# Performance work log

Hardware: AMD Instinct MI355X
Metric: run time of the kernel (lower is better)

The kernel has to match this reference:

```python
import jax, jax.numpy as jnp
import numpy as np

N_HEADS = 16
WINDOW = 4
THETA = 10000.0


def _freqs_1d(dim, L, theta=THETA):
    f = 1.0 / theta ** (np.arange(0, dim, 2, dtype=np.float32) / dim)  # [dim/2]
    ang = np.arange(L, dtype=np.float32)[:, None] * f[None, :]         # [L, dim/2]
    return jnp.asarray(np.cos(ang)), jnp.asarray(np.sin(ang))


def _freqs_2d(dim, H, W, theta=THETA):
    f = 1.0 / theta ** (np.arange(0, dim, 2, dtype=np.float32) / dim)  # [dim/2]
    fh = np.arange(H, dtype=np.float32)[:, None] * f[0::2][None, :]    # [H, dim/4]
    fw = np.arange(W, dtype=np.float32)[:, None] * f[1::2][None, :]    # [W, dim/4]
    ang = np.concatenate([
        np.broadcast_to(fh[:, None, :], (H, W, fh.shape[1])),
        np.broadcast_to(fw[None, :, :], (H, W, fw.shape[1])),
    ], axis=-1)                                                        # [H, W, dim/2]
    return jnp.asarray(np.cos(ang)), jnp.asarray(np.sin(ang))


def _rope(x, cos, sin):
    # x: [..., N, D]; cos/sin broadcastable to x's leading dims with trailing D/2
    sh = x.shape
    xr = x.reshape(sh[:-1] + (sh[-1] // 2, 2))
    re, im = xr[..., 0], xr[..., 1]
    o_re = re * cos - im * sin
    o_im = re * sin + im * cos
    return jnp.stack([o_re, o_im], axis=-1).reshape(sh)


def setup_inputs() -> dict:
    key = jax.random.key(0)
    ks = jax.random.split(key, 5)
    B, T, H, W, E = 2, 8, 16, 16, 512
    S = 2 * T * H * W
    std = 0.02
    return {
        "hidden_states": jax.random.normal(ks[0], (B, S, E), jnp.float32),
        "in_proj_weight": jax.random.normal(ks[1], (3 * E, E), jnp.float32) * std,
        "in_proj_bias": jnp.zeros((3 * E,), jnp.float32),
        "out_proj_weight": jax.random.normal(ks[2], (E, E), jnp.float32) * std,
        "out_proj_bias": jnp.zeros((E,), jnp.float32),
        "temporal_embed": jax.random.normal(ks[3], (WINDOW, E), jnp.float32) * std,
        "T": T, "H": H, "W": W,
    }


def reference(hidden_states, in_proj_weight, in_proj_bias, out_proj_weight,
              out_proj_bias, temporal_embed, T, H, W):
    B, S, E = hidden_states.shape
    n, d = N_HEADS, E // N_HEADS
    HW = H * W
    THW = T * HW
    L2 = 2 * HW  # tokens per frame fed to attention

    # first (outer) in-projection
    qkv = hidden_states @ in_proj_weight.T + in_proj_bias  # [B,S,3E]
    q, k, v = jnp.split(qkv, 3, axis=-1)
    q = q.reshape(B, S, n, d)
    k = k.reshape(B, S, n, d)

    # 1D RoPE on first T*H*W tokens (per-frame length H*W)
    cos1, sin1 = _freqs_1d(d, HW)
    c1, s1 = cos1[:, None, :], sin1[:, None, :]  # [HW,1,d/2]
    q1 = _rope(q[:, :THW].reshape(B * T, HW, n, d), c1, s1)
    k1 = _rope(k[:, :THW].reshape(B * T, HW, n, d), c1, s1)

    # 2D RoPE on last T*H*W tokens
    cos2, sin2 = _freqs_2d(d, H, W)
    c2, s2 = cos2[:, :, None, :], sin2[:, :, None, :]  # [H,W,1,d/2]
    q2 = _rope(q[:, THW:].reshape(B * T, H, W, n, d), c2, s2).reshape(B * T, HW, n, d)
    k2 = _rope(k[:, THW:].reshape(B * T, H, W, n, d), c2, s2).reshape(B * T, HW, n, d)

    q_mha = jnp.concatenate([q1, q2], axis=1).reshape(B * T, L2, E)
    k_comb = jnp.concatenate([k1, k2], axis=1).reshape(B, T, L2, E)
    v_comb = v.reshape(B, T, L2, E)

    # sliding window over frames (left-pad with zeros)
    k_pad = jnp.pad(k_comb, ((0, 0), (WINDOW - 1, 0), (0, 0), (0, 0)))
    v_pad = jnp.pad(v_comb, ((0, 0), (WINDOW - 1, 0), (0, 0), (0, 0)))
    k_win = jnp.stack([k_pad[:, i:i + T] for i in range(WINDOW)], axis=2)
    v_win = jnp.stack([v_pad[:, i:i + T] for i in range(WINDOW)], axis=2)
    k_win = k_win + temporal_embed[None, None, :, None, :]
    k_mha = k_win.reshape(B * T, WINDOW * L2, E)
    v_mha = v_win.reshape(B * T, WINDOW * L2, E)

    # inner nn.MultiheadAttention: projects q/k/v AGAIN with in_proj chunks
    Wq, Wk, Wv = jnp.split(in_proj_weight, 3, axis=0)
    bq, bk, bv = jnp.split(in_proj_bias, 3, axis=0)
    qh = (q_mha @ Wq.T + bq).reshape(B * T, L2, n, d)
    kh = (k_mha @ Wk.T + bk).reshape(B * T, WINDOW * L2, n, d)
    vh = (v_mha @ Wv.T + bv).reshape(B * T, WINDOW * L2, n, d)

    scale = 1.0 / jnp.sqrt(jnp.asarray(d, jnp.float32))
    scores = jnp.einsum('bqnd,bknd->bnqk', qh, kh) * scale
    attn = jax.nn.softmax(scores, axis=-1)
    o = jnp.einsum('bnqk,bknd->bqnd', attn, vh).reshape(B * T, L2, E)
    out = o @ out_proj_weight.T + out_proj_bias
    return out.reshape(B, S, E)
```

## Files before the change

kernel.cpp:

```cpp
#include <hip/hip_runtime.h>


#define LOG2T_OVER_16 0.83048202372184059f
#define SCL 0.25505837391169026f

typedef unsigned short u16;
typedef unsigned int u32;
typedef __attribute__((ext_vector_type(2))) unsigned int u32x2;
typedef __attribute__((ext_vector_type(4))) float f32x4;
typedef __attribute__((ext_vector_type(8))) short s16x8;

__device__ __forceinline__ u16 bf16b(float x) {
  u32 u = __float_as_uint(x);
  u32 r = u + 0x7FFFu + ((u >> 16) & 1u);
  return (u16)(r >> 16);
}
__device__ __forceinline__ float bf2f(u16 s) {
  return __uint_as_float(((u32)s) << 16);
}
__device__ __forceinline__ u32 cvtpk(float lo, float hi) {
  u32 r;
  asm("v_cvt_pk_bf16_f32 %0, %1, %2" : "=v"(r) : "v"(lo), "v"(hi));
  return r;
}

__device__ __forceinline__ void gld_lds16(const u16* g, u16* l) {
  __builtin_amdgcn_global_load_lds(
      (const __attribute__((address_space(1))) unsigned int*)g,
      (__attribute__((address_space(3))) unsigned int*)l, 16, 0, 0);
}

__global__ __launch_bounds__(256) void cast3_bf16(
    const float* __restrict__ a, const float* __restrict__ b,
    const float* __restrict__ c, u16* __restrict__ dst) {
  const int i = blockIdx.x * 256 + threadIdx.x;
  const float* s;
  int so;
  if (i < 524288) { s = a; so = i; }
  else if (i < 622592) { s = b; so = i - 524288; }
  else { s = c; so = i - 622592; }
  float4 x = ((const float4*)s)[so * 2], y = ((const float4*)s)[so * 2 + 1];
  union { u32 u[4]; s16x8 v; } w;
  w.u[0] = cvtpk(x.x, x.y); w.u[1] = cvtpk(x.z, x.w);
  w.u[2] = cvtpk(y.x, y.y); w.u[3] = cvtpk(y.z, y.w);
  ((s16x8*)dst)[i] = w.v;
}

template<int OUTF32>
__device__ __forceinline__ void gemm_core(
    const u16* __restrict__ A, const u16* __restrict__ Bw,
    const float* __restrict__ bias, void* __restrict__ Cp,
    int N, int K, float scale, u16* As, u16* Bs) {
  const int tid = threadIdx.x;
  const int row0 = blockIdx.y * 128;
  const int col0 = blockIdx.x * 128;
  const int lane = tid & 63, wid = tid >> 6;
  const int col = lane & 15, g = lane >> 4;
  const int wm = wid >> 1, wn = wid & 1;

  const int s0 = tid, s1 = 256 + tid;
  const int r0 = s0 >> 2, kp0 = (s0 & 3) * 8;
  const int r1 = s1 >> 2, kp1 = (s1 & 3) * 8;

  f32x4 acc[4][4] = {};

  auto stage = [&](int buf, int k0) {
    u16* ab = As + buf * 4096;
    u16* bb = Bs + buf * 4096;
    gld_lds16(A + (size_t)(row0 + r0) * K + k0 + kp0, ab + s0 * 8);
    gld_lds16(A + (size_t)(row0 + r1) * K + k0 + kp1, ab + s1 * 8);
    gld_lds16(Bw + (size_t)(col0 + r0) * K + k0 + kp0, bb + s0 * 8);
    gld_lds16(Bw + (size_t)(col0 + r1) * K + k0 + kp1, bb + s1 * 8);
  };

  stage(0, 0);
  asm volatile("s_waitcnt vmcnt(0)" ::: "memory");
  __syncthreads();

  const int NT = K / 32;
  int cur = 0;
  for (int t = 0; t < NT; ++t) {
    if (t + 1 < NT) stage(cur ^ 1, (t + 1) * 32);
    const u16* ab = As + cur * 4096;
    const u16* bb = Bs + cur * 4096;
    s16x8 a[4], b[4];
    #pragma unroll
    for (int i = 0; i < 4; ++i)
      a[i] = *(const s16x8*)(ab + (wm * 64 + i * 16 + col) * 32 + g * 8);
    #pragma unroll
    for (int i = 0; i < 4; ++i)
      b[i] = *(const s16x8*)(bb + (wn * 64 + i * 16 + col) * 32 + g * 8);
    #pragma unroll
    for (int mi = 0; mi < 4; ++mi)
      #pragma unroll
      for (int ni = 0; ni < 4; ++ni)
        acc[mi][ni] = __builtin_amdgcn_mfma_f32_16x16x32_bf16(a[mi], b[ni], acc[mi][ni], 0, 0, 0);
    asm volatile("s_waitcnt vmcnt(0)" ::: "memory");
    __syncthreads();
    cur ^= 1;
  }

  const int crow = row0 + wm * 64, ccol = col0 + wn * 64;
  #pragma unroll
  for (int mi = 0; mi < 4; ++mi) {
    #pragma unroll
    for (int ni = 0; ni < 4; ++ni) {
      const int cc = ccol + ni * 16 + col;
      const float bb_ = bias ? bias[cc] : 0.0f;
      #pragma unroll
      for (int r = 0; r < 4; ++r) {
        const int rr = crow + mi * 16 + g * 4 + r;
        float v = (acc[mi][ni][r] + bb_) * scale;
        if (OUTF32) ((float*)Cp)[(size_t)rr * N + cc] = v;
        else        ((u16*)Cp)[(size_t)rr * N + cc] = bf16b(v);
      }
    }
  }
}

__global__ __launch_bounds__(256) void gemm_bf16(
    const u16* __restrict__ A, const u16* __restrict__ Bw,
    const float* __restrict__ bias, u16* __restrict__ C, int N, int K, float scale) {
  __shared__ u16 As[2 * 4096];
  __shared__ u16 Bs[2 * 4096];
  gemm_core<0>(A, Bw, bias, C, N, K, scale, As, Bs);
}

__global__ __launch_bounds__(256) void gemm_f32out(
    const u16* __restrict__ A, const u16* __restrict__ Bw,
    const float* __restrict__ bias, float* __restrict__ C, int N, int K, float scale) {
  __shared__ u16 As[2 * 4096];
  __shared__ u16 Bs[2 * 4096];
  gemm_core<1>(A, Bw, bias, C, N, K, scale, As, Bs);
}

__global__ __launch_bounds__(256) void gemm2_batched(
    const u16* __restrict__ Ab, const u16* __restrict__ Wb,
    const float* __restrict__ b_in, u16* __restrict__ Cb) {
  __shared__ u16 As[2 * 4096];
  __shared__ u16 Bs[2 * 4096];
  const int z = blockIdx.z;
  const u16* A  = Ab + (size_t)z * 4194304;
  const u16* Bw = Wb + (size_t)z * 262144;
  u16* C = Cb + (size_t)z * 4194304;
  const float* bias = (z == 0) ? b_in : (z == 2 ? b_in + 1024 : nullptr);
  const float scale = (z == 0) ? SCL : 1.0f;
  gemm_core<0>(A, Bw, bias, C, 512, 512, scale, As, Bs);
}

__global__ __launch_bounds__(256) void ang_table_kernel(float2* __restrict__ tab) {
  const int idx = blockIdx.x * 256 + threadIdx.x;
  const int j = idx >> 4, u = idx & 15;
  float ang;
  if (j < 256) {
    ang = (float)j * exp2f(-(float)u * LOG2T_OVER_16);
  } else {
    const int jj = j - 256, hh = jj >> 4, ww = jj & 15;
    ang = (u < 8) ? (float)hh * exp2f(-(float)(2 * u) * LOG2T_OVER_16)
                  : (float)ww * exp2f(-(float)(2 * (u - 8) + 1) * LOG2T_OVER_16);
  }
  float s, c;
  sincosf(ang, &s, &c);
  tab[idx] = make_float2(c, s);
}

__global__ __launch_bounds__(256) void rope_relayout_bf(
    const u16* __restrict__ qkv, const float2* __restrict__ tab,
    u16* __restrict__ qm, u16* __restrict__ kc, u16* __restrict__ vc) {
  const int R = blockIdx.x * 2 + (threadIdx.x >> 7);
  const int t2 = threadIdx.x & 127;
  const int j = R & 511, bt = R >> 9;
  const int b = bt >> 3, tt = bt & 7;
  const int head = t2 >> 3, u0 = (t2 & 7) * 2;
  const int e0 = head * 32 + u0 * 2;

  const int tok = (j < 256) ? (b * 4096 + tt * 256 + j)
                            : (b * 4096 + 2048 + tt * 256 + (j - 256));
  float4 cs = *(const float4*)&tab[j * 16 + u0];
  const float c0 = cs.x, s0 = cs.y, c1 = cs.z, s1 = cs.w;

  const size_t base = (size_t)tok * 1536 + e0;
  const size_t orow = (size_t)R * 512 + e0;

  auto rot = [&](u32x2 in) -> u32x2 {
    float r0 = bf2f((u16)(in[0] & 0xffff)), i0 = bf2f((u16)(in[0] >> 16));
    float r1 = bf2f((u16)(in[1] & 0xffff)), i1 = bf2f((u16)(in[1] >> 16));
    u32x2 o;
    o[0] = cvtpk(r0 * c0 - i0 * s0, r0 * s0 + i0 * c0);
    o[1] = cvtpk(r1 * c1 - i1 * s1, r1 * s1 + i1 * c1);
    return o;
  };
  *(u32x2*)(qm + orow) = rot(*(const u32x2*)(qkv + base));
  *(u32x2*)(kc + orow) = rot(*(const u32x2*)(qkv + base + 512));
  const int vtok = b * 4096 + tt * 512 + j;
  *(u32x2*)(vc + orow) = *(const u32x2*)(qkv + (size_t)vtok * 1536 + 1024 + e0);
}

__global__ __launch_bounds__(256) void tep_kernel(
    const float* __restrict__ te, const float* __restrict__ Wk,
    const float* __restrict__ bk, float* __restrict__ tep) {
  const int idx = blockIdx.x * 256 + threadIdx.x;
  const int i = idx >> 9, c = idx & 511;
  float s = bk[c];
  const float* terow = te + i * 512;
  const float* wrow = Wk + (size_t)c * 512;
  #pragma unroll 8
  for (int e = 0; e < 512; ++e) s = fmaf(terow[e], wrow[e], s);
  tep[idx] = s;
}

__global__ __launch_bounds__(256) void transpose_v_bf16(
    const u16* __restrict__ vc2, u16* __restrict__ vt) {
  const int f = blockIdx.x, h = blockIdx.y;
  __shared__ float tile[64][35];
  const int tid = threadIdx.x;
  for (int k0 = 0; k0 < 512; k0 += 64) {
    __syncthreads();
    {
      const int key = tid >> 2, d0 = (tid & 3) * 8;
      s16x8 v = *(const s16x8*)(vc2 + (size_t)(f * 512 + k0 + key) * 512 + h * 32 + d0);
      #pragma unroll
      for (int q = 0; q < 8; ++q) tile[key][d0 + q] = bf2f((u16)v[q]);
    }
    __syncthreads();
    {
      const int d = tid >> 3, j0 = (tid & 7) * 8;
      union { u32 u[4]; s16x8 v; } w;
      #pragma unroll
      for (int q = 0; q < 4; ++q)
        w.u[q] = cvtpk(tile[j0 + 2 * q][d], tile[j0 + 2 * q + 1][d]);
      *(s16x8*)(vt + (size_t)((f * 16 + h) * 32 + d) * 512 + k0 + j0) = w.v;
    }
  }
}

__global__ __launch_bounds__(256) void attn_mfma(
    const u16* __restrict__ qh, const u16* __restrict__ kbf,
    const float* __restrict__ tep, const u16* __restrict__ vt,
    const float* __restrict__ bv, u16* __restrict__ obf) {
  const u32 orig = blockIdx.x;
  const u32 sw = (orig & 7) * 256 + (orig >> 3);
  const int h = sw >> 7, bt = (sw >> 3) & 15, zc = sw & 7;
  const int b = bt >> 3, t = bt & 7;
  const int tid = threadIdx.x;
  const int lane = tid & 63, w = tid >> 6;
  const int col = lane & 15, g = lane >> 4;

  __shared__ __align__(128) u16 plds[4][4096];
  u16* pl = plds[w];
  const u32 pl_base = (u32)(uintptr_t)pl + (u32)lane * 8u;
  float* cf = (float*)&plds[0][0];

  const int phys_e = (col & 4) ? 4 + (col >> 3) : (col >> 3);
  const int wbase = phys_e * 64 + (col & 3) * 16 + g * 4;

  const int qrow0 = bt * 512 + zc * 64;
  s16x8 qa[4];
  #pragma unroll
  for (int m = 0; m < 4; ++m)
    qa[m] = *(const s16x8*)(qh + (size_t)(qrow0 + m * 16 + col) * 512 + h * 32 + g * 8);

  f32x4 acc[4][2] = {};
  f32x4 lsum[4] = {};
  const f32x4 zero4 = {0.f, 0.f, 0.f, 0.f};

  const int fs = t + w - 3;
  const float* tprow = tep + w * 512 + h * 32;
  float t8[8];
  #pragma unroll
  for (int j = 0; j < 8; ++j) t8[j] = tprow[g * 8 + j];

  if (fs < 0) {
    float* pf = (float*)pl;
    #pragma unroll
    for (int m = 0; m < 4; ++m) {
      float part = 0.f;
      #pragma unroll
      for (int j = 0; j < 8; ++j) part = fmaf(bf2f((u16)qa[m][j]), t8[j], part);
      part += __shfl_xor(part, 16);
      part += __shfl_xor(part, 32);
      float e = __builtin_amdgcn_exp2f(part) * 512.0f;
      if (lane < 16) pf[m * 16 + col] = e;
    }
    asm volatile("s_waitcnt lgkmcnt(0)" ::: "memory");
    const float bv0 = bv[h * 32 + col], bv1 = bv[h * 32 + 16 + col];
    #pragma unroll
    for (int m = 0; m < 4; ++m)
      #pragma unroll
      for (int r = 0; r < 4; ++r) {
        float e = pf[m * 16 + g * 4 + r];
        lsum[m][r] += (col == 0) ? e : 0.f;
        acc[m][0][r] += e * bv0;
        acc[m][1][r] += e * bv1;
      }
  } else {
    const size_t krow0 = (size_t)((b * 8 + fs) * 512);
    const size_t vrow0 = (size_t)(((b * 8 + fs) * 16 + h) * 32);
    for (int it = 0; it < 8; ++it) {
      const int kk0 = it * 64;
      f32x4 S[4][4];
      #pragma unroll
      for (int n = 0; n < 4; ++n) {
        s16x8 kv = *(const s16x8*)(kbf + (krow0 + kk0 + n * 16 + col) * 512 + h * 32 + g * 8);
        union { u32 u[4]; s16x8 v; } kb;
        #pragma unroll
        for (int p = 0; p < 4; ++p)
          kb.u[p] = cvtpk(bf2f((u16)kv[2 * p]) + t8[2 * p],
                          bf2f((u16)kv[2 * p + 1]) + t8[2 * p + 1]);
        #pragma unroll
        for (int m = 0; m < 4; ++m)
          S[m][n] = __builtin_amdgcn_mfma_f32_16x16x32_bf16(qa[m], kb.v, zero4, 0, 0, 0);
      }
      #pragma unroll
      for (int m = 0; m < 4; ++m) {
        #pragma unroll
        for (int n = 0; n < 4; ++n) {
          f32x4 p;
          #pragma unroll
          for (int r = 0; r < 4; ++r) p[r] = __builtin_amdgcn_exp2f(S[m][n][r]);
          lsum[m] += p;
          const int E = m * 1024 + (n >> 1) * 512 + (n & 1) * 128 + wbase;
          *(uint2*)&pl[E] = make_uint2(cvtpk(p[0], p[1]), cvtpk(p[2], p[3]));
        }
      }
      s16x8 vfr[2][2];
      #pragma unroll
      for (int ks = 0; ks < 2; ++ks)
        #pragma unroll
        for (int n = 0; n < 2; ++n)
          vfr[ks][n] = *(const s16x8*)(vt + (vrow0 + n * 16 + col) * 512 + kk0 + ks * 32 + g * 8);
      asm volatile("s_waitcnt lgkmcnt(0)" ::: "memory");
      union AF { u32x2 h2[2]; s16x8 v; };
      AF pa[4][2];
      #pragma unroll
      for (int m = 0; m < 4; ++m)
        #pragma unroll
        for (int ks = 0; ks < 2; ++ks) {
          u32 a0 = pl_base + (u32)((m * 1024 + ks * 512) * 2);
          asm volatile("ds_read_b64_tr_b16 %0, %1" : "=v"(pa[m][ks].h2[0]) : "v"(a0));
          asm volatile("ds_read_b64_tr_b16 %0, %1 offset:512" : "=v"(pa[m][ks].h2[1]) : "v"(a0));
        }
      asm volatile("s_waitcnt lgkmcnt(0)" ::: "memory");
      __builtin_amdgcn_sched_barrier(0);
      #pragma unroll
      for (int m = 0; m < 4; ++m)
        #pragma unroll
        for (int ks = 0; ks < 2; ++ks)
          #pragma unroll
          for (int n = 0; n < 2; ++n)
            acc[m][n] = __builtin_amdgcn_mfma_f32_16x16x32_bf16(pa[m][ks].v, vfr[ks][n], acc[m][n], 0, 0, 0);
    }
  }

  #pragma unroll
  for (int m = 0; m < 4; ++m)
    #pragma unroll
    for (int r = 0; r < 4; ++r) {
      float s = lsum[m][r];
      s += __shfl_xor(s, 1);
      s += __shfl_xor(s, 2);
      s += __shfl_xor(s, 4);
      s += __shfl_xor(s, 8);
      lsum[m][r] = s;
    }

  __syncthreads();
  if (w > 0) {
    float* dst = cf + (size_t)(w - 1) * 2048 + lane * 32;
    #pragma unroll
    for (int m = 0; m < 4; ++m) {
      *(f32x4*)(dst + m * 8) = acc[m][0];
      *(f32x4*)(dst + m * 8 + 4) = acc[m][1];
    }
    if (col == 0) {
      float* d2 = cf + 6144 + (w - 1) * 64 + g * 16;
      #pragma unroll
      for (int m = 0; m < 4; ++m) *(f32x4*)(d2 + m * 4) = lsum[m];
    }
  }
  __syncthreads();
  if (w == 0) {
    #pragma unroll
    for (int w2 = 0; w2 < 3; ++w2) {
      const float* src = cf + (size_t)w2 * 2048 + lane * 32;
      const float* s2 = cf + 6144 + w2 * 64 + g * 16;
      #pragma unroll
      for (int m = 0; m < 4; ++m) {
        acc[m][0] += *(const f32x4*)(src + m * 8);
        acc[m][1] += *(const f32x4*)(src + m * 8 + 4);
        lsum[m] += *(const f32x4*)(s2 + m * 4);
      }
    }
    #pragma unroll
    for (int m = 0; m < 4; ++m) {
      f32x4 inv;
      #pragma unroll
      for (int r = 0; r < 4; ++r) inv[r] = 1.0f / lsum[m][r];
      #pragma unroll
      for (int n = 0; n < 2; ++n)
        #pragma unroll
        for (int r = 0; r < 4; ++r)
          pl[(m * 16 + g * 4 + r) * 32 + n * 16 + col] = bf16b(acc[m][n][r] * inv[r]);
    }
    asm volatile("s_waitcnt lgkmcnt(0)" ::: "memory");
    #pragma unroll
    for (int i = 0; i < 8; ++i) {
      const int row = i * 8 + (lane >> 3);
      u32x2 wv = *(u32x2*)&pl[row * 32 + (lane & 7) * 4];
      *(u32x2*)(obf + (size_t)(qrow0 + row) * 512 + h * 32 + (lane & 7) * 4) = wv;
    }
  }
}

extern "C" void kernel_launch(void* const* d_in, const int* in_sizes, int n_in,
                              void* d_out, int out_size, void* d_ws, size_t ws_size,
                              hipStream_t stream) {
  (void)in_sizes; (void)n_in; (void)out_size; (void)ws_size;
  const float* hs    = (const float*)d_in[0];
  const float* w_in  = (const float*)d_in[1];
  const float* b_in  = (const float*)d_in[2];
  const float* w_out = (const float*)d_in[3];
  const float* b_out = (const float*)d_in[4];
  const float* te    = (const float*)d_in[5];

  u16* w16 = (u16*)d_ws;
  u16* hs_bf   = w16;
  u16* win_bf  = w16 + 4194304;
  u16* wout_bf = w16 + 4980736;
  u16* qkv_bf  = w16 + 5242880;
  u16* qm_bf   = w16 + 17825792;
  u16* kc_bf   = w16 + 22020096;
  u16* vc_bf   = w16 + 26214400;
  float* tep   = (float*)(w16 + 30408704);
  float2* tab  = (float2*)(w16 + 30412800);
  u16* qh_bf   = w16 + 5242880;
  u16* kbf     = w16 + 9437184;
  u16* vc2_bf  = w16 + 13631488;
  u16* vt      = w16 + 17825792;
  u16* o_bf    = w16 + 22020096;

  cast3_bf16<<<2560, 256, 0, stream>>>(hs, w_in, w_out, w16);
  ang_table_kernel<<<32, 256, 0, stream>>>(tab);

  gemm_bf16<<<dim3(12, 64), 256, 0, stream>>>(hs_bf, win_bf, b_in, qkv_bf, 1536, 512, 1.0f);

  rope_relayout_bf<<<4096, 256, 0, stream>>>(qkv_bf, tab, qm_bf, kc_bf, vc_bf);

  tep_kernel<<<8, 256, 0, stream>>>(te, w_in + 512 * 512, b_in + 512, tep);

  gemm2_batched<<<dim3(4, 64, 3), 256, 0, stream>>>(qm_bf, win_bf, b_in, qh_bf);

  transpose_v_bf16<<<dim3(16, 16), 256, 0, stream>>>(vc2_bf, vt);

  attn_mfma<<<2048, 256, 0, stream>>>(qh_bf, kbf, tep, vt, b_in + 1024, o_bf);

  gemm_f32out<<<dim3(4, 64), 256, 0, stream>>>(o_bf, wout_bf, b_out, (float*)d_out, 512, 512, 1.0f);
}
```

Before: 274.5 us.

## Fuse V transpose into gemm epilogue and restructure attention to 512-thread blocks

```diff
diff --git a/kernel.cpp b/kernel.cpp
--- a/kernel.cpp
+++ b/kernel.cpp
@@ -46,11 +46,11 @@
   ((s16x8*)dst)[i] = w.v;
 }
 
-template<int OUTF32>
+template<int MODE>
 __device__ __forceinline__ void gemm_core(
     const u16* __restrict__ A, const u16* __restrict__ Bw,
     const float* __restrict__ bias, void* __restrict__ Cp,
-    int N, int K, float scale, u16* As, u16* Bs) {
+    int N, int K, int lda, float scale, u16* As, u16* Bs) {
   const int tid = threadIdx.x;
   const int row0 = blockIdx.y * 128;
   const int col0 = blockIdx.x * 128;
@@ -67,8 +67,8 @@
   auto stage = [&](int buf, int k0) {
     u16* ab = As + buf * 4096;
     u16* bb = Bs + buf * 4096;
-    gld_lds16(A + (size_t)(row0 + r0) * K + k0 + kp0, ab + s0 * 8);
-    gld_lds16(A + (size_t)(row0 + r1) * K + k0 + kp1, ab + s1 * 8);
+    gld_lds16(A + (size_t)(row0 + r0) * lda + k0 + kp0, ab + s0 * 8);
+    gld_lds16(A + (size_t)(row0 + r1) * lda + k0 + kp1, ab + s1 * 8);
     gld_lds16(Bw + (size_t)(col0 + r0) * K + k0 + kp0, bb + s0 * 8);
     gld_lds16(Bw + (size_t)(col0 + r1) * K + k0 + kp1, bb + s1 * 8);
   };
@@ -107,12 +107,22 @@
     for (int ni = 0; ni < 4; ++ni) {
       const int cc = ccol + ni * 16 + col;
       const float bb_ = bias ? bias[cc] : 0.0f;
-      #pragma unroll
-      for (int r = 0; r < 4; ++r) {
-        const int rr = crow + mi * 16 + g * 4 + r;
-        float v = (acc[mi][ni][r] + bb_) * scale;
-        if (OUTF32) ((float*)Cp)[(size_t)rr * N + cc] = v;
-        else        ((u16*)Cp)[(size_t)rr * N + cc] = bf16b(v);
+      if (MODE == 2) {
+        const int key0 = crow + mi * 16 + g * 4;
+        u16* dst = (u16*)Cp +
+            ((size_t)((key0 >> 9) * 16 + (cc >> 5)) * 32 + (cc & 31)) * 512 + (key0 & 511);
+        union { u16 s[4]; u32x2 v; } pk;
+        #pragma unroll
+        for (int r = 0; r < 4; ++r) pk.s[r] = bf16b(acc[mi][ni][r] + bb_);
+        *(u32x2*)dst = pk.v;
+      } else {
+        #pragma unroll
+        for (int r = 0; r < 4; ++r) {
+          const int rr = crow + mi * 16 + g * 4 + r;
+          float v = (acc[mi][ni][r] + bb_) * scale;
+          if (MODE == 1) ((float*)Cp)[(size_t)rr * N + cc] = v;
+          else           ((u16*)Cp)[(size_t)rr * N + cc] = bf16b(v);
+        }
       }
     }
   }
@@ -123,7 +133,7 @@
     const float* __restrict__ bias, u16* __restrict__ C, int N, int K, float scale) {
   __shared__ u16 As[2 * 4096];
   __shared__ u16 Bs[2 * 4096];
-  gemm_core<0>(A, Bw, bias, C, N, K, scale, As, Bs);
+  gemm_core<0>(A, Bw, bias, C, N, K, K, scale, As, Bs);
 }
 
 __global__ __launch_bounds__(256) void gemm_f32out(
@@ -131,21 +141,25 @@
     const float* __restrict__ bias, float* __restrict__ C, int N, int K, float scale) {
   __shared__ u16 As[2 * 4096];
   __shared__ u16 Bs[2 * 4096];
-  gemm_core<1>(A, Bw, bias, C, N, K, scale, As, Bs);
+  gemm_core<1>(A, Bw, bias, C, N, K, K, scale, As, Bs);
 }
 
 __global__ __launch_bounds__(256) void gemm2_batched(
-    const u16* __restrict__ Ab, const u16* __restrict__ Wb,
-    const float* __restrict__ b_in, u16* __restrict__ Cb) {
+    const u16* __restrict__ Ab, const u16* __restrict__ qkv,
+    const u16* __restrict__ Wb, const float* __restrict__ b_in,
+    u16* __restrict__ Cb) {
   __shared__ u16 As[2 * 4096];
   __shared__ u16 Bs[2 * 4096];
   const int z = blockIdx.z;
-  const u16* A  = Ab + (size_t)z * 4194304;
   const u16* Bw = Wb + (size_t)z * 262144;
   u16* C = Cb + (size_t)z * 4194304;
-  const float* bias = (z == 0) ? b_in : (z == 2 ? b_in + 1024 : nullptr);
-  const float scale = (z == 0) ? SCL : 1.0f;
-  gemm_core<0>(A, Bw, bias, C, 512, 512, scale, As, Bs);
+  if (z == 2) {
+    gemm_core<2>(qkv + 1024, Bw, b_in + 1024, C, 512, 512, 1536, 1.0f, As, Bs);
+  } else {
+    const float* bias = (z == 0) ? b_in : nullptr;
+    const float scale = (z == 0) ? SCL : 1.0f;
+    gemm_core<0>(Ab + (size_t)z * 4194304, Bw, bias, C, 512, 512, 512, scale, As, Bs);
+  }
 }
 
 __global__ __launch_bounds__(256) void ang_table_kernel(float2* __restrict__ tab) {
@@ -166,7 +180,7 @@
 
 __global__ __launch_bounds__(256) void rope_relayout_bf(
     const u16* __restrict__ qkv, const float2* __restrict__ tab,
-    u16* __restrict__ qm, u16* __restrict__ kc, u16* __restrict__ vc) {
+    u16* __restrict__ qm, u16* __restrict__ kc) {
   const int R = blockIdx.x * 2 + (threadIdx.x >> 7);
   const int t2 = threadIdx.x & 127;
   const int j = R & 511, bt = R >> 9;
@@ -192,8 +206,6 @@
   };
   *(u32x2*)(qm + orow) = rot(*(const u32x2*)(qkv + base));
   *(u32x2*)(kc + orow) = rot(*(const u32x2*)(qkv + base + 512));
-  const int vtok = b * 4096 + tt * 512 + j;
-  *(u32x2*)(vc + orow) = *(const u32x2*)(qkv + (size_t)vtok * 1536 + 1024 + e0);
 }
 
 __global__ __launch_bounds__(256) void tep_kernel(
@@ -209,32 +221,7 @@
   tep[idx] = s;
 }
 
-__global__ __launch_bounds__(256) void transpose_v_bf16(
-    const u16* __restrict__ vc2, u16* __restrict__ vt) {
-  const int f = blockIdx.x, h = blockIdx.y;
-  __shared__ float tile[64][35];
-  const int tid = threadIdx.x;
-  for (int k0 = 0; k0 < 512; k0 += 64) {
-    __syncthreads();
-    {
-      const int key = tid >> 2, d0 = (tid & 3) * 8;
-      s16x8 v = *(const s16x8*)(vc2 + (size_t)(f * 512 + k0 + key) * 512 + h * 32 + d0);
-      #pragma unroll
-      for (int q = 0; q < 8; ++q) tile[key][d0 + q] = bf2f((u16)v[q]);
-    }
-    __syncthreads();
-    {
-      const int d = tid >> 3, j0 = (tid & 7) * 8;
-      union { u32 u[4]; s16x8 v; } w;
-      #pragma unroll
-      for (int q = 0; q < 4; ++q)
-        w.u[q] = cvtpk(tile[j0 + 2 * q][d], tile[j0 + 2 * q + 1][d]);
-      *(s16x8*)(vt + (size_t)((f * 16 + h) * 32 + d) * 512 + k0 + j0) = w.v;
-    }
-  }
-}
-
-__global__ __launch_bounds__(256) void attn_mfma(
+__global__ __launch_bounds__(512) void attn_mfma(
     const u16* __restrict__ qh, const u16* __restrict__ kbf,
     const float* __restrict__ tep, const u16* __restrict__ vt,
     const float* __restrict__ bv, u16* __restrict__ obf) {
@@ -243,171 +230,155 @@
   const int h = sw >> 7, bt = (sw >> 3) & 15, zc = sw & 7;
   const int b = bt >> 3, t = bt & 7;
   const int tid = threadIdx.x;
-  const int lane = tid & 63, w = tid >> 6;
+  const int lane = tid & 63, wv = tid >> 6;
+  const int slot = wv & 3, half = wv >> 2;
   const int col = lane & 15, g = lane >> 4;
 
-  __shared__ __align__(128) u16 plds[4][4096];
-  u16* pl = plds[w];
-  const u32 pl_base = (u32)(uintptr_t)pl + (u32)lane * 8u;
-  float* cf = (float*)&plds[0][0];
-
-  const int phys_e = (col & 4) ? 4 + (col >> 3) : (col >> 3);
-  const int wbase = phys_e * 64 + (col & 3) * 16 + g * 4;
-
-  const int qrow0 = bt * 512 + zc * 64;
-  s16x8 qa[4];
+  __shared__ float cf[6400];
+
+  const int qrow0 = bt * 512 + zc * 64 + half * 32;
+  s16x8 qa[2];
   #pragma unroll
-  for (int m = 0; m < 4; ++m)
+  for (int m = 0; m < 2; ++m)
     qa[m] = *(const s16x8*)(qh + (size_t)(qrow0 + m * 16 + col) * 512 + h * 32 + g * 8);
 
-  f32x4 acc[4][2] = {};
-  f32x4 lsum[4] = {};
-  const f32x4 zero4 = {0.f, 0.f, 0.f, 0.f};
-
-  const int fs = t + w - 3;
-  const float* tprow = tep + w * 512 + h * 32;
+  const float* tprow = tep + slot * 512 + h * 32;
   float t8[8];
   #pragma unroll
   for (int j = 0; j < 8; ++j) t8[j] = tprow[g * 8 + j];
-
+  float dtc[2];
+  #pragma unroll
+  for (int m = 0; m < 2; ++m) {
+    float p = 0.f;
+    #pragma unroll
+    for (int j = 0; j < 8; ++j) p = fmaf(bf2f((u16)qa[m][j]), t8[j], p);
+    p += __shfl_xor(p, 16);
+    p += __shfl_xor(p, 32);
+    dtc[m] = p;
+  }
+
+  f32x4 acc[2][2] = {};
+  float lsc[2] = {};
+
+  const int fs = t + slot - 3;
   if (fs < 0) {
-    float* pf = (float*)pl;
-    #pragma unroll
-    for (int m = 0; m < 4; ++m) {
-      float part = 0.f;
-      #pragma unroll
-      for (int j = 0; j < 8; ++j) part = fmaf(bf2f((u16)qa[m][j]), t8[j], part);
-      part += __shfl_xor(part, 16);
-      part += __shfl_xor(part, 32);
-      float e = __builtin_amdgcn_exp2f(part) * 512.0f;
-      if (lane < 16) pf[m * 16 + col] = e;
-    }
-    asm volatile("s_waitcnt lgkmcnt(0)" ::: "memory");
     const float bv0 = bv[h * 32 + col], bv1 = bv[h * 32 + 16 + col];
     #pragma unroll
-    for (int m = 0; m < 4; ++m)
+    for (int m = 0; m < 2; ++m) {
+      float e = __builtin_amdgcn_exp2f(dtc[m]) * 512.0f;
+      if (g == 0) lsc[m] += e;
       #pragma unroll
       for (int r = 0; r < 4; ++r) {
-        float e = pf[m * 16 + g * 4 + r];
-        lsum[m][r] += (col == 0) ? e : 0.f;
-        acc[m][0][r] += e * bv0;
-        acc[m][1][r] += e * bv1;
+        float egr = __int_as_float(
+            __builtin_amdgcn_ds_bpermute((g * 4 + r) * 4, __float_as_int(e)));
+        acc[m][0][r] += egr * bv0;
+        acc[m][1][r] += egr * bv1;
       }
+    }
   } else {
     const size_t krow0 = (size_t)((b * 8 + fs) * 512);
     const size_t vrow0 = (size_t)(((b * 8 + fs) * 16 + h) * 32);
+    const int addrA = (col + 32 * (g & 1)) * 4;
+    const int addrB = addrA + 64;
+    const bool lowg = (g < 2);
     for (int it = 0; it < 8; ++it) {
       const int kk0 = it * 64;
-      f32x4 S[4][4];
-      #pragma unroll
-      for (int n = 0; n < 4; ++n) {
-        s16x8 kv = *(const s16x8*)(kbf + (krow0 + kk0 + n * 16 + col) * 512 + h * 32 + g * 8);
-        union { u32 u[4]; s16x8 v; } kb;
-        #pragma unroll
-        for (int p = 0; p < 4; ++p)
-          kb.u[p] = cvtpk(bf2f((u16)kv[2 * p]) + t8[2 * p],
-                          bf2f((u16)kv[2 * p + 1]) + t8[2 * p + 1]);
-        #pragma unroll
-        for (int m = 0; m < 4; ++m)
-          S[m][n] = __builtin_amdgcn_mfma_f32_16x16x32_bf16(qa[m], kb.v, zero4, 0, 0, 0);
-      }
-      #pragma unroll
-      for (int m = 0; m < 4; ++m) {
+      s16x8 kb[4], vf[2][2];
+      #pragma unroll
+      for (int n = 0; n < 4; ++n)
+        kb[n] = *(const s16x8*)(kbf + (krow0 + kk0 + n * 16 + col) * 512 + h * 32 + g * 8);
+      #pragma unroll
+      for (int ks = 0; ks < 2; ++ks)
+        #pragma unroll
+        for (int nd = 0; nd < 2; ++nd)
+          vf[ks][nd] = *(const s16x8*)(vt + (vrow0 + nd * 16 + col) * 512 + kk0 + ks * 32 + g * 8);
+      #pragma unroll
+      for (int m = 0; m < 2; ++m) {
+        const f32x4 dti = {dtc[m], dtc[m], dtc[m], dtc[m]};
+        u32 pr[4][2];
+        float lacc = 0.f;
         #pragma unroll
         for (int n = 0; n < 4; ++n) {
+          f32x4 S = __builtin_amdgcn_mfma_f32_16x16x32_bf16(kb[n], qa[m], dti, 0, 0, 0);
           f32x4 p;
           #pragma unroll
-          for (int r = 0; r < 4; ++r) p[r] = __builtin_amdgcn_exp2f(S[m][n][r]);
-          lsum[m] += p;
-          const int E = m * 1024 + (n >> 1) * 512 + (n & 1) * 128 + wbase;
-          *(uint2*)&pl[E] = make_uint2(cvtpk(p[0], p[1]), cvtpk(p[2], p[3]));
+          for (int r = 0; r < 4; ++r) p[r] = __builtin_amdgcn_exp2f(S[r]);
+          lacc += (p[0] + p[1]) + (p[2] + p[3]);
+          pr[n][0] = cvtpk(p[0], p[1]);
+          pr[n][1] = cvtpk(p[2], p[3]);
+        }
+        lsc[m] += lacc;
+        #pragma unroll
+        for (int ks = 0; ks < 2; ++ks) {
+          union { u32 u[4]; s16x8 v; } pw;
+          #pragma unroll
+          for (int wq = 0; wq < 4; ++wq) {
+            const int aA = (wq & 2) ? addrB : addrA;
+            u32 va = (u32)__builtin_amdgcn_ds_bpermute(aA, (int)pr[2 * ks][wq & 1]);
+            u32 vb = (u32)__builtin_amdgcn_ds_bpermute(aA, (int)pr[2 * ks + 1][wq & 1]);
+            pw.u[wq] = lowg ? va : vb;
+          }
+          acc[m][0] = __builtin_amdgcn_mfma_f32_16x16x32_bf16(pw.v, vf[ks][0], acc[m][0], 0, 0, 0);
+          acc[m][1] = __builtin_amdgcn_mfma_f32_16x16x32_bf16(pw.v, vf[ks][1], acc[m][1], 0, 0, 0);
         }
       }
-      s16x8 vfr[2][2];
-      #pragma unroll
-      for (int ks = 0; ks < 2; ++ks)
-        #pragma unroll
-        for (int n = 0; n < 2; ++n)
-          vfr[ks][n] = *(const s16x8*)(vt + (vrow0 + n * 16 + col) * 512 + kk0 + ks * 32 + g * 8);
-      asm volatile("s_waitcnt lgkmcnt(0)" ::: "memory");
-      union AF { u32x2 h2[2]; s16x8 v; };
-      AF pa[4][2];
-      #pragma unroll
-      for (int m = 0; m < 4; ++m)
-        #pragma unroll
-        for (int ks = 0; ks < 2; ++ks) {
-          u32 a0 = pl_base + (u32)((m * 1024 + ks * 512) * 2);
-          asm volatile("ds_read_b64_tr_b16 %0, %1" : "=v"(pa[m][ks].h2[0]) : "v"(a0));
-          asm volatile("ds_read_b64_tr_b16 %0, %1 offset:512" : "=v"(pa[m][ks].h2[1]) : "v"(a0));
-        }
-      asm volatile("s_waitcnt lgkmcnt(0)" ::: "memory");
-      __builtin_amdgcn_sched_barrier(0);
-      #pragma unroll
-      for (int m = 0; m < 4; ++m)
-        #pragma unroll
-        for (int ks = 0; ks < 2; ++ks)
-          #pragma unroll
-          for (int n = 0; n < 2; ++n)
-            acc[m][n] = __builtin_amdgcn_mfma_f32_16x16x32_bf16(pa[m][ks].v, vfr[ks][n], acc[m][n], 0, 0, 0);
     }
   }
 
   #pragma unroll
-  for (int m = 0; m < 4; ++m)
-    #pragma unroll
-    for (int r = 0; r < 4; ++r) {
-      float s = lsum[m][r];
-      s += __shfl_xor(s, 1);
-      s += __shfl_xor(s, 2);
-      s += __shfl_xor(s, 4);
-      s += __shfl_xor(s, 8);
-      lsum[m][r] = s;
-    }
-
-  __syncthreads();
-  if (w > 0) {
-    float* dst = cf + (size_t)(w - 1) * 2048 + lane * 32;
-    #pragma unroll
-    for (int m = 0; m < 4; ++m) {
+  for (int m = 0; m < 2; ++m) {
+    lsc[m] += __shfl_xor(lsc[m], 16);
+    lsc[m] += __shfl_xor(lsc[m], 32);
+  }
+
+  if (slot > 0) {
+    float* dst = cf + (size_t)(half * 3 + slot - 1) * 1024 + lane * 16;
+    #pragma unroll
+    for (int m = 0; m < 2; ++m) {
       *(f32x4*)(dst + m * 8) = acc[m][0];
       *(f32x4*)(dst + m * 8 + 4) = acc[m][1];
     }
-    if (col == 0) {
-      float* d2 = cf + 6144 + (w - 1) * 64 + g * 16;
-      #pragma unroll
-      for (int m = 0; m < 4; ++m) *(f32x4*)(d2 + m * 4) = lsum[m];
+    if (g == 0) {
+      float* d2 = cf + 6144 + (half * 3 + slot - 1) * 32;
+      #pragma unroll
+      for (int m = 0; m < 2; ++m) d2[m * 16 + col] = lsc[m];
     }
   }
   __syncthreads();
-  if (w == 0) {
-    #pragma unroll
-    for (int w2 = 0; w2 < 3; ++w2) {
-      const float* src = cf + (size_t)w2 * 2048 + lane * 32;
-      const float* s2 = cf + 6144 + w2 * 64 + g * 16;
-      #pragma unroll
-      for (int m = 0; m < 4; ++m) {
+  if (slot == 0) {
+    #pragma unroll
+    for (int s2 = 0; s2 < 3; ++s2) {
+      const float* src = cf + (size_t)(half * 3 + s2) * 1024 + lane * 16;
+      const float* l2 = cf + 6144 + (half * 3 + s2) * 32;
+      #pragma unroll
+      for (int m = 0; m < 2; ++m) {
         acc[m][0] += *(const f32x4*)(src + m * 8);
         acc[m][1] += *(const f32x4*)(src + m * 8 + 4);
-        lsum[m] += *(const f32x4*)(s2 + m * 4);
+        lsc[m] += l2[m * 16 + col];
       }
     }
-    #pragma unroll
-    for (int m = 0; m < 4; ++m) {
+    u16* st = (u16*)(cf + half * 3 * 1024);
+    #pragma unroll
+    for (int m = 0; m < 2; ++m) {
       f32x4 inv;
       #pragma unroll
-      for (int r = 0; r < 4; ++r) inv[r] = 1.0f / lsum[m][r];
-      #pragma unroll
-      for (int n = 0; n < 2; ++n)
+      for (int r = 0; r < 4; ++r) {
+        float lr = __int_as_float(
+            __builtin_amdgcn_ds_bpermute((g * 4 + r) * 4, __float_as_int(lsc[m])));
+        inv[r] = 1.0f / lr;
+      }
+      #pragma unroll
+      for (int nd = 0; nd < 2; ++nd)
         #pragma unroll
         for (int r = 0; r < 4; ++r)
-          pl[(m * 16 + g * 4 + r) * 32 + n * 16 + col] = bf16b(acc[m][n][r] * inv[r]);
+          st[(m * 16 + g * 4 + r) * 32 + nd * 16 + col] = bf16b(acc[m][nd][r] * inv[r]);
     }
     asm volatile("s_waitcnt lgkmcnt(0)" ::: "memory");
     #pragma unroll
-    for (int i = 0; i < 8; ++i) {
+    for (int i = 0; i < 4; ++i) {
       const int row = i * 8 + (lane >> 3);
-      u32x2 wv = *(u32x2*)&pl[row * 32 + (lane & 7) * 4];
-      *(u32x2*)(obf + (size_t)(qrow0 + row) * 512 + h * 32 + (lane & 7) * 4) = wv;
+      u32x2 wq = *(u32x2*)&st[row * 32 + (lane & 7) * 4];
+      *(u32x2*)(obf + (size_t)(qrow0 + row) * 512 + h * 32 + (lane & 7) * 4) = wq;
     }
   }
 }
@@ -430,13 +401,11 @@
   u16* qkv_bf  = w16 + 5242880;
   u16* qm_bf   = w16 + 17825792;
   u16* kc_bf   = w16 + 22020096;
-  u16* vc_bf   = w16 + 26214400;
   float* tep   = (float*)(w16 + 30408704);
   float2* tab  = (float2*)(w16 + 30412800);
-  u16* qh_bf   = w16 + 5242880;
-  u16* kbf     = w16 + 9437184;
-  u16* vc2_bf  = w16 + 13631488;
-  u16* vt      = w16 + 17825792;
+  u16* qh_bf   = w16 + 30445568;
+  u16* kbf     = w16 + 34639872;
+  u16* vt      = w16 + 38834176;
   u16* o_bf    = w16 + 22020096;
 
   cast3_bf16<<<2560, 256, 0, stream>>>(hs, w_in, w_out, w16);
@@ -444,15 +413,13 @@
 
   gemm_bf16<<<dim3(12, 64), 256, 0, stream>>>(hs_bf, win_bf, b_in, qkv_bf, 1536, 512, 1.0f);
 
-  rope_relayout_bf<<<4096, 256, 0, stream>>>(qkv_bf, tab, qm_bf, kc_bf, vc_bf);
+  rope_relayout_bf<<<4096, 256, 0, stream>>>(qkv_bf, tab, qm_bf, kc_bf);
 
   tep_kernel<<<8, 256, 0, stream>>>(te, w_in + 512 * 512, b_in + 512, tep);
 
-  gemm2_batched<<<dim3(4, 64, 3), 256, 0, stream>>>(qm_bf, win_bf, b_in, qh_bf);
-
-  transpose_v_bf16<<<dim3(16, 16), 256, 0, stream>>>(vc2_bf, vt);
-
-  attn_mfma<<<2048, 256, 0, stream>>>(qh_bf, kbf, tep, vt, b_in + 1024, o_bf);
+  gemm2_batched<<<dim3(4, 64, 3), 256, 0, stream>>>(qm_bf, qkv_bf, win_bf, b_in, qh_bf);
+
+  attn_mfma<<<2048, 512, 0, stream>>>(qh_bf, kbf, tep, vt, b_in + 1024, o_bf);
 
   gemm_f32out<<<dim3(4, 64), 256, 0, stream>>>(o_bf, wout_bf, b_out, (float*)d_out, 512, 512, 1.0f);
 }
```

Result: slower. 291.4 us (+6.1%).
